# Performance work log

Hardware: AMD Instinct MI355X
Metric: run time of the kernel (lower is better)

## Reference

```python
import jax, jax.numpy as jnp
import numpy as np

N_NODES = 100000
N_EDGES = 1600000
MSG = 128
EPS = 1e-12  # F.normalize default eps


def setup_inputs() -> dict:
    key = jax.random.key(0)
    ks = jax.random.split(key, 12)
    s = 1.0 / np.sqrt(MSG)
    inp = {
        "x": jax.random.normal(ks[0], (N_NODES, 3), dtype=jnp.float32),
        "m_ij": jax.random.normal(ks[1], (N_EDGES, MSG), dtype=jnp.float32),
        "edges": jax.random.randint(ks[2], (2, N_EDGES), 0, N_NODES, dtype=jnp.int64),
        # weigths MLP: Linear(MSG,MSG) -> SiLU -> Linear(MSG,1)
        "Ww1": jax.random.uniform(ks[3], (MSG, MSG), jnp.float32, -s, s),
        "bw1": jax.random.uniform(ks[4], (MSG,), jnp.float32, -s, s),
        "Ww2": jax.random.uniform(ks[5], (MSG, 1), jnp.float32, -s, s),
        "bw2": jax.random.uniform(ks[6], (1,), jnp.float32, -s, s),
        # attention MLP: Linear(MSG,MSG) -> SiLU -> Linear(MSG,1)
        "Wa1": jax.random.uniform(ks[7], (MSG, MSG), jnp.float32, -s, s),
        "ba1": jax.random.uniform(ks[8], (MSG,), jnp.float32, -s, s),
        "Wa2": jax.random.uniform(ks[9], (MSG, 1), jnp.float32, -s, s),
        "ba2": jax.random.uniform(ks[10], (1,), jnp.float32, -s, s),
    }
    return inp


def reference(x, m_ij, edges, Ww1, bw1, Ww2, bw2, Wa1, ba1, Wa2, ba2):
    n_nodes = x.shape[0]
    src = edges[0]  # receiver index (scatter target)
    dst = edges[1]  # neighbor index

    # w_ij = MLP(m_ij) -> [E, 1]
    w_ij = jax.nn.silu(m_ij @ Ww1 + bw1) @ Ww2 + bw2

    # attention: a_ij = exp(MLP(m_ij)); normalized per receiver node (softmax-like)
    a_ij = jnp.exp(jax.nn.silu(m_ij @ Wa1 + ba1) @ Wa2 + ba2)  # [E, 1]
    a_i = jax.ops.segment_sum(a_ij, src, num_segments=n_nodes)  # [N, 1]
    w_ij = w_ij * (a_ij / a_i[src])

    # normalized position differences, weighted
    d = x[dst] - x[src]  # [E, 3]
    norm = jnp.maximum(jnp.linalg.norm(d, axis=1, keepdims=True), EPS)
    x_ij = (d / norm) * w_ij

    x_diff = jax.ops.segment_sum(x_ij, src, num_segments=n_nodes)  # [N, 3]
    return x + x_diff
```

## Files before the change

### kernel.cpp

```cpp
#include <hip/hip_runtime.h>
#include <cmath>

#define MSG 128
#define TILE 32
#define TPB 256
#define NB_MAX 768

typedef __attribute__((ext_vector_type(8))) __bf16 bf16x8;
typedef __attribute__((ext_vector_type(4))) float f32x4;

__device__ __forceinline__ unsigned short f2bf(float f) {
  union { float f; unsigned u; } v; v.f = f;
  unsigned r = v.u + 0x7FFFu + ((v.u >> 16) & 1u);
  return (unsigned short)(r >> 16);
}

__global__ void prep_weights_kernel(const float* __restrict__ Ww1,
                                    const float* __restrict__ Wa1,
                                    unsigned short* __restrict__ WtW,
                                    unsigned short* __restrict__ WtA) {
  int idx = blockIdx.x * blockDim.x + threadIdx.x;
  if (idx < MSG * MSG) {
    int k = idx >> 7;
    int n = idx & 127;
    WtW[n * MSG + k] = f2bf(Ww1[idx]);
    WtA[n * MSG + k] = f2bf(Wa1[idx]);
  }
}

__device__ __forceinline__ void gload_lds16(const float* g, float* l) {
  __builtin_amdgcn_global_load_lds(
      (const __attribute__((address_space(1))) void*)g,
      (__attribute__((address_space(3))) void*)l, 16, 0, 0);
}

__global__ __launch_bounds__(TPB, 3)
void edge_mlp_pipe_kernel(const float* __restrict__ m_ij,
                          const unsigned short* __restrict__ WtW,
                          const unsigned short* __restrict__ WtA,
                          const float* __restrict__ bw1, const float* __restrict__ Ww2,
                          const float* __restrict__ bw2,
                          const float* __restrict__ ba1, const float* __restrict__ Wa2,
                          const float* __restrict__ ba2,
                          const int* __restrict__ src,
                          const int* __restrict__ dst,
                          const float* __restrict__ x,
                          float* __restrict__ num4, int E, int ntiles) {
  __shared__ __align__(16) float buf[2][TILE * MSG];
  __shared__ float plds[2][4][TILE];

  const int tid = threadIdx.x;
  const int w = tid >> 6;
  const int lane = tid & 63;
  const int quad = lane >> 4;
  const int l16 = lane & 15;

  bf16x8 wf[2][2][4];
  f32x4 c1[2][2], c2[2][2];
  #pragma unroll
  for (int nt = 0; nt < 2; ++nt) {
    const int unit16 = w * 32 + nt * 16;
    const size_t ro = (size_t)(unit16 + l16) * MSG + quad * 8;
    #pragma unroll
    for (int kt = 0; kt < 4; ++kt) {
      wf[nt][0][kt] = *(const bf16x8*)(WtW + ro + kt * 32);
      wf[nt][1][kt] = *(const bf16x8*)(WtA + ro + kt * 32);
    }
    const int co = unit16 + quad * 4;
    c1[nt][0] = *(const f32x4*)(bw1 + co);
    c2[nt][0] = *(const f32x4*)(Ww2 + co);
    c1[nt][1] = *(const f32x4*)(ba1 + co);
    c2[nt][1] = *(const f32x4*)(Wa2 + co);
  }
  const float bw2s = bw2[0], ba2s = ba2[0];

  auto stage = [&](int tile, int bsel) {
    #pragma unroll
    for (int i = 0; i < 4; ++i) {
      const int chunk = i * TPB + tid;
      const int db = chunk * 16;
      const int row = db >> 9;
      const int col = db & 511;
      const int scol = col ^ ((row & 7) << 4);
      int grow = tile * TILE + row;
      if (grow >= E) grow = E - 1;
      gload_lds16(m_ij + (size_t)grow * MSG + (scol >> 2), &buf[bsel][0] + (db >> 2));
    }
  };

  const int fid = w * 8 + (lane & 7);

  int tt = blockIdx.x;
  int ge = tt * TILE + fid;
  bool vcur = (ge < E);
  int gec = vcur ? ge : 0;
  int sN = src[gec];
  int dN = dst[gec];
  asm volatile("" ::: "memory");
  stage(tt, 0);
  asm volatile("s_waitcnt vmcnt(4)" ::: "memory");
  float sx = x[3 * sN], sy = x[3 * sN + 1], sz = x[3 * sN + 2];
  float gx = x[3 * dN], gy = x[3 * dN + 1], gz = x[3 * dN + 2];
  asm volatile("s_waitcnt vmcnt(6)" ::: "memory");
  __builtin_amdgcn_s_barrier();
  int cur = 0;

  for (; tt < ntiles; tt += gridDim.x) {
    const int nxt = tt + (int)gridDim.x;
    const int snxt = (nxt < ntiles) ? nxt : (ntiles - 1);

    const int geN = snxt * TILE + fid;
    const bool vnxt = (geN < E);
    const int geNc = vnxt ? geN : 0;
    const int sN2 = src[geNc];
    const int dN2 = dst[geNc];
    asm volatile("" ::: "memory");
    stage(snxt, cur ^ 1);

    #pragma unroll
    for (int et = 0; et < 2; ++et) {
      const int row = et * 16 + l16;
      const int rbase = row * MSG;
      const int xorf = (row & 7) << 2;
      bf16x8 bfv[4];
      #pragma unroll
      for (int kt = 0; kt < 4; ++kt) {
        const int c0 = quad * 8 + kt * 32;
        const f32x4 v0 = *(const f32x4*)(&buf[cur][rbase + (c0 ^ xorf)]);
        const f32x4 v1 = *(const f32x4*)(&buf[cur][rbase + ((c0 + 4) ^ xorf)]);
        bf16x8 f;
        f[0] = (__bf16)v0.x; f[1] = (__bf16)v0.y;
        f[2] = (__bf16)v0.z; f[3] = (__bf16)v0.w;
        f[4] = (__bf16)v1.x; f[5] = (__bf16)v1.y;
        f[6] = (__bf16)v1.z; f[7] = (__bf16)v1.w;
        bfv[kt] = f;
      }
      f32x4 acc[2][2];
      #pragma unroll
      for (int nt = 0; nt < 2; ++nt) {
        acc[nt][0] = {0.f, 0.f, 0.f, 0.f};
        acc[nt][1] = {0.f, 0.f, 0.f, 0.f};
      }
      #pragma unroll
      for (int kt = 0; kt < 4; ++kt) {
        #pragma unroll
        for (int nt = 0; nt < 2; ++nt) {
          acc[nt][0] = __builtin_amdgcn_mfma_f32_16x16x32_bf16(wf[nt][0][kt], bfv[kt], acc[nt][0], 0, 0, 0);
          acc[nt][1] = __builtin_amdgcn_mfma_f32_16x16x32_bf16(wf[nt][1][kt], bfv[kt], acc[nt][1], 0, 0, 0);
        }
      }
      float pW = 0.f, pA = 0.f;
      #pragma unroll
      for (int nt = 0; nt < 2; ++nt) {
        #pragma unroll
        for (int r = 0; r < 4; ++r) {
          const float hw = acc[nt][0][r] + c1[nt][0][r];
          const float ha = acc[nt][1][r] + c1[nt][1][r];
          pW += (hw * c2[nt][0][r]) * __builtin_amdgcn_rcpf(1.f + __expf(-hw));
          pA += (ha * c2[nt][1][r]) * __builtin_amdgcn_rcpf(1.f + __expf(-ha));
        }
      }
      pW += __shfl_xor(pW, 16, 64); pW += __shfl_xor(pW, 32, 64);
      pA += __shfl_xor(pA, 16, 64); pA += __shfl_xor(pA, 32, 64);
      if (quad == 0) {
        plds[0][w][et * 16 + l16] = pW;
        plds[1][w][et * 16 + l16] = pA;
      }
    }

    asm volatile("s_waitcnt lgkmcnt(0)" ::: "memory");
    __builtin_amdgcn_s_barrier();

    asm volatile("s_waitcnt vmcnt(6)" ::: "memory");

    {
      float sW = 0.f, sA = 0.f;
      #pragma unroll
      for (int ww = 0; ww < 4; ++ww) {
        sW += plds[0][ww][fid];
        sA += plds[1][ww][fid];
      }
      const float a = __expf(sA + ba2s);
      const float t = (sW + bw2s) * a;
      const float dx = gx - sx, dy = gy - sy, dz = gz - sz;
      const float nrm = sqrtf(dx * dx + dy * dy + dz * dz);
      const float inv = t * __builtin_amdgcn_rcpf(fmaxf(nrm, 1e-12f));
      const float m = vcur ? 1.f : 0.f;
      if (quad == 0 && l16 < 8) {
        float* basep = num4 + (size_t)4 * sN;
        atomicAdd(basep + 0, dx * inv * m);
        atomicAdd(basep + 1, dy * inv * m);
        atomicAdd(basep + 2, dz * inv * m);
        atomicAdd(basep + 3, a * m);
      }
    }

    asm volatile("s_waitcnt vmcnt(8)" ::: "memory");
    const float sx2 = x[3 * sN2], sy2 = x[3 * sN2 + 1], sz2 = x[3 * sN2 + 2];
    const float gx2 = x[3 * dN2], gy2 = x[3 * dN2 + 1], gz2 = x[3 * dN2 + 2];

    asm volatile("s_waitcnt vmcnt(10) lgkmcnt(0)" ::: "memory");
    __builtin_amdgcn_s_barrier();

    sN = sN2; dN = dN2; vcur = vnxt;
    sx = sx2; sy = sy2; sz = sz2;
    gx = gx2; gy = gy2; gz = gz2;
    cur ^= 1;
  }
}

__global__ void finalize_kernel(const float* __restrict__ x,
                                const f32x4* __restrict__ num4,
                                float* __restrict__ out, int N) {
  int n = blockIdx.x * blockDim.x + threadIdx.x;
  if (n >= N) return;
  const f32x4 v = num4[n];
  const float inv = (v[3] != 0.f) ? __builtin_amdgcn_rcpf(v[3]) : 0.f;
  out[3 * n + 0] = x[3 * n + 0] + v[0] * inv;
  out[3 * n + 1] = x[3 * n + 1] + v[1] * inv;
  out[3 * n + 2] = x[3 * n + 2] + v[2] * inv;
}

extern "C" void kernel_launch(void* const* d_in, const int* in_sizes, int n_in,
                              void* d_out, int out_size, void* d_ws, size_t ws_size,
                              hipStream_t stream) {
  const float* x    = (const float*)d_in[0];
  const float* m_ij = (const float*)d_in[1];
  const int*   edges = (const int*)d_in[2];
  const float* Ww1 = (const float*)d_in[3];
  const float* bw1 = (const float*)d_in[4];
  const float* Ww2 = (const float*)d_in[5];
  const float* bw2 = (const float*)d_in[6];
  const float* Wa1 = (const float*)d_in[7];
  const float* ba1 = (const float*)d_in[8];
  const float* Wa2 = (const float*)d_in[9];
  const float* ba2 = (const float*)d_in[10];

  const int N = in_sizes[0] / 3;
  const int E = in_sizes[1] / MSG;
  const int* src = edges;
  const int* dst = edges + E;

  char* p = (char*)d_ws;
  unsigned short* WtW = (unsigned short*)p; p += (size_t)MSG * MSG * 2;
  unsigned short* WtA = (unsigned short*)p; p += (size_t)MSG * MSG * 2;
  float* num4 = (float*)p; p += (size_t)N * 4 * 4;

  float* out = (float*)d_out;

  const int ntiles = (E + TILE - 1) / TILE;
  const int nb = ntiles < NB_MAX ? ntiles : NB_MAX;

  hipMemsetAsync(num4, 0, (size_t)N * 4 * 4, stream);
  prep_weights_kernel<<<(MSG * MSG + 255) / 256, 256, 0, stream>>>(Ww1, Wa1, WtW, WtA);
  edge_mlp_pipe_kernel<<<nb, TPB, 0, stream>>>(
      m_ij, WtW, WtA, bw1, Ww2, bw2, ba1, Wa2, ba2, src, dst, x, num4, E, ntiles);
  finalize_kernel<<<(N + 255) / 256, 256, 0, stream>>>(x, (const f32x4*)num4, out, N);
}
```

Baseline: 1.204 ms.

## Software-pipeline MFMA and SiLU epilogue across tiles with triple-buffered LDS

Restructures the persistent edge loop so the MFMA for tile i runs after the barrier, while the SiLU/reduction epilogue of tile i-1 runs before it, and the node scatter is deferred by one iteration. LDS staging moves from double to triple buffering with a two-tile lookahead, and bias/second-layer weights move from registers to LDS. The aim is to overlap the transcendental-heavy epilogue with matrix work and memory latency and to hide more load latency. In exchange it uses more LDS and registers, which may lower occupancy, and the remaining vmcnt waits are loosely chosen.

```diff
diff --git a/kernel.cpp b/kernel.cpp
--- a/kernel.cpp
+++ b/kernel.cpp
@@ -46,35 +46,36 @@
                           const int* __restrict__ dst,
                           const float* __restrict__ x,
                           float* __restrict__ num4, int E, int ntiles) {
-  __shared__ __align__(16) float buf[2][TILE * MSG];
+  __shared__ __align__(16) float buf[3][TILE * MSG];
   __shared__ float plds[2][4][TILE];
+  __shared__ float clds[2][2][MSG];
 
   const int tid = threadIdx.x;
   const int w = tid >> 6;
   const int lane = tid & 63;
   const int quad = lane >> 4;
   const int l16 = lane & 15;
+  const int G = (int)gridDim.x;
+
+  for (int e = tid; e < 512; e += TPB) {
+    const int mat = e >> 8, c = (e >> 7) & 1, u = e & 127;
+    const float* s = (mat == 0) ? (c == 0 ? bw1 : Ww2) : (c == 0 ? ba1 : Wa2);
+    clds[mat][c][u] = s[u];
+  }
 
   bf16x8 wf[2][2][4];
-  f32x4 c1[2][2], c2[2][2];
   #pragma unroll
   for (int nt = 0; nt < 2; ++nt) {
-    const int unit16 = w * 32 + nt * 16;
-    const size_t ro = (size_t)(unit16 + l16) * MSG + quad * 8;
+    const size_t ro = (size_t)(w * 32 + nt * 16 + l16) * MSG + quad * 8;
     #pragma unroll
     for (int kt = 0; kt < 4; ++kt) {
       wf[nt][0][kt] = *(const bf16x8*)(WtW + ro + kt * 32);
       wf[nt][1][kt] = *(const bf16x8*)(WtA + ro + kt * 32);
     }
-    const int co = unit16 + quad * 4;
-    c1[nt][0] = *(const f32x4*)(bw1 + co);
-    c2[nt][0] = *(const f32x4*)(Ww2 + co);
-    c1[nt][1] = *(const f32x4*)(ba1 + co);
-    c2[nt][1] = *(const f32x4*)(Wa2 + co);
   }
   const float bw2s = bw2[0], ba2s = ba2[0];
 
-  auto stage = [&](int tile, int bsel) {
+  auto stage = [&](int tile, float* base) {
     #pragma unroll
     for (int i = 0; i < 4; ++i) {
       const int chunk = i * TPB + tid;
@@ -84,80 +85,69 @@
       const int scol = col ^ ((row & 7) << 4);
       int grow = tile * TILE + row;
       if (grow >= E) grow = E - 1;
-      gload_lds16(m_ij + (size_t)grow * MSG + (scol >> 2), &buf[bsel][0] + (db >> 2));
+      gload_lds16(m_ij + (size_t)grow * MSG + (scol >> 2), base + (db >> 2));
     }
   };
 
   const int fid = w * 8 + (lane & 7);
 
-  int tt = blockIdx.x;
-  int ge = tt * TILE + fid;
-  bool vcur = (ge < E);
-  int gec = vcur ? ge : 0;
-  int sN = src[gec];
-  int dN = dst[gec];
-  asm volatile("" ::: "memory");
-  stage(tt, 0);
-  asm volatile("s_waitcnt vmcnt(4)" ::: "memory");
-  float sx = x[3 * sN], sy = x[3 * sN + 1], sz = x[3 * sN + 2];
-  float gx = x[3 * dN], gy = x[3 * dN + 1], gz = x[3 * dN + 2];
-  asm volatile("s_waitcnt vmcnt(6)" ::: "memory");
-  __builtin_amdgcn_s_barrier();
-  int cur = 0;
-
-  for (; tt < ntiles; tt += gridDim.x) {
-    const int nxt = tt + (int)gridDim.x;
-    const int snxt = (nxt < ntiles) ? nxt : (ntiles - 1);
-
-    const int geN = snxt * TILE + fid;
-    const bool vnxt = (geN < E);
-    const int geNc = vnxt ? geN : 0;
+  int fsN[2] = {0, 0};
+  float fm[2] = {0.f, 0.f};
+  float fX[2][6];
+  #pragma unroll
+  for (int k = 0; k < 6; ++k) { fX[0][k] = 0.f; fX[1][k] = 0.f; }
+
+  f32x4 pacc[8];
+  #pragma unroll
+  for (int k = 0; k < 8; ++k) pacc[k] = {0.f, 0.f, 0.f, 0.f};
+
+  const int t0 = blockIdx.x;
+  {
+    int ge = t0 * TILE + fid;
+    bool v = (ge < E);
+    int gec = v ? ge : 0;
+    int sN = src[gec], dN = dst[gec];
+    stage(t0, &buf[0][0]);
+    { int t1 = t0 + G; if (t1 >= ntiles) t1 = ntiles - 1; stage(t1, &buf[1][0]); }
+    fsN[1] = sN; fm[1] = v ? 1.f : 0.f;
+    fX[1][0] = x[3 * sN]; fX[1][1] = x[3 * sN + 1]; fX[1][2] = x[3 * sN + 2];
+    fX[1][3] = x[3 * dN]; fX[1][4] = x[3 * dN + 1]; fX[1][5] = x[3 * dN + 2];
+    __syncthreads();
+  }
+
+  int p = 0;
+  int ci = 0;
+
+  for (int tt = t0; tt < ntiles; tt += G) {
+    int tn = tt + G;
+    const bool tnok = tn < ntiles;
+    const int tnc = tnok ? tn : ntiles - 1;
+    const int geN = tnc * TILE + fid;
+    const bool vN = tnok && (geN < E);
+    const int geNc = vN ? geN : 0;
     const int sN2 = src[geNc];
     const int dN2 = dst[geNc];
-    asm volatile("" ::: "memory");
-    stage(snxt, cur ^ 1);
+
+    { int ts = tt + 2 * G; if (ts >= ntiles) ts = ntiles - 1;
+      int sb = ci + 2; if (sb >= 3) sb -= 3;
+      stage(ts, &buf[sb][0]); }
 
     #pragma unroll
     for (int et = 0; et < 2; ++et) {
-      const int row = et * 16 + l16;
-      const int rbase = row * MSG;
-      const int xorf = (row & 7) << 2;
-      bf16x8 bfv[4];
-      #pragma unroll
-      for (int kt = 0; kt < 4; ++kt) {
-        const int c0 = quad * 8 + kt * 32;
-        const f32x4 v0 = *(const f32x4*)(&buf[cur][rbase + (c0 ^ xorf)]);
-        const f32x4 v1 = *(const f32x4*)(&buf[cur][rbase + ((c0 + 4) ^ xorf)]);
-        bf16x8 f;
-        f[0] = (__bf16)v0.x; f[1] = (__bf16)v0.y;
-        f[2] = (__bf16)v0.z; f[3] = (__bf16)v0.w;
-        f[4] = (__bf16)v1.x; f[5] = (__bf16)v1.y;
-        f[6] = (__bf16)v1.z; f[7] = (__bf16)v1.w;
-        bfv[kt] = f;
-      }
-      f32x4 acc[2][2];
-      #pragma unroll
-      for (int nt = 0; nt < 2; ++nt) {
-        acc[nt][0] = {0.f, 0.f, 0.f, 0.f};
-        acc[nt][1] = {0.f, 0.f, 0.f, 0.f};
-      }
-      #pragma unroll
-      for (int kt = 0; kt < 4; ++kt) {
-        #pragma unroll
-        for (int nt = 0; nt < 2; ++nt) {
-          acc[nt][0] = __builtin_amdgcn_mfma_f32_16x16x32_bf16(wf[nt][0][kt], bfv[kt], acc[nt][0], 0, 0, 0);
-          acc[nt][1] = __builtin_amdgcn_mfma_f32_16x16x32_bf16(wf[nt][1][kt], bfv[kt], acc[nt][1], 0, 0, 0);
-        }
-      }
       float pW = 0.f, pA = 0.f;
       #pragma unroll
       for (int nt = 0; nt < 2; ++nt) {
+        const int co = w * 32 + nt * 16 + quad * 4;
+        const f32x4 b1w = *(const f32x4*)&clds[0][0][co];
+        const f32x4 w2w = *(const f32x4*)&clds[0][1][co];
+        const f32x4 b1a = *(const f32x4*)&clds[1][0][co];
+        const f32x4 w2a = *(const f32x4*)&clds[1][1][co];
         #pragma unroll
         for (int r = 0; r < 4; ++r) {
-          const float hw = acc[nt][0][r] + c1[nt][0][r];
-          const float ha = acc[nt][1][r] + c1[nt][1][r];
-          pW += (hw * c2[nt][0][r]) * __builtin_amdgcn_rcpf(1.f + __expf(-hw));
-          pA += (ha * c2[nt][1][r]) * __builtin_amdgcn_rcpf(1.f + __expf(-ha));
+          const float hw = pacc[et * 4 + nt * 2 + 0][r] + b1w[r];
+          const float ha = pacc[et * 4 + nt * 2 + 1][r] + b1a[r];
+          pW += (hw * w2w[r]) * __builtin_amdgcn_rcpf(1.f + __expf(-hw));
+          pA += (ha * w2a[r]) * __builtin_amdgcn_rcpf(1.f + __expf(-ha));
         }
       }
       pW += __shfl_xor(pW, 16, 64); pW += __shfl_xor(pW, 32, 64);
@@ -171,41 +161,119 @@
     asm volatile("s_waitcnt lgkmcnt(0)" ::: "memory");
     __builtin_amdgcn_s_barrier();
 
-    asm volatile("s_waitcnt vmcnt(6)" ::: "memory");
-
     {
-      float sW = 0.f, sA = 0.f;
+      const float* bufc = &buf[ci][0];
       #pragma unroll
-      for (int ww = 0; ww < 4; ++ww) {
-        sW += plds[0][ww][fid];
-        sA += plds[1][ww][fid];
-      }
+      for (int et = 0; et < 2; ++et) {
+        const int row = et * 16 + l16;
+        const int rbase = row * MSG;
+        const int xorf = (row & 7) << 2;
+        bf16x8 bfv[4];
+        #pragma unroll
+        for (int kt = 0; kt < 4; ++kt) {
+          const int c0 = quad * 8 + kt * 32;
+          const f32x4 v0 = *(const f32x4*)(bufc + rbase + (c0 ^ xorf));
+          const f32x4 v1 = *(const f32x4*)(bufc + rbase + ((c0 + 4) ^ xorf));
+          bf16x8 f;
+          f[0] = (__bf16)v0.x; f[1] = (__bf16)v0.y;
+          f[2] = (__bf16)v0.z; f[3] = (__bf16)v0.w;
+          f[4] = (__bf16)v1.x; f[5] = (__bf16)v1.y;
+          f[6] = (__bf16)v1.z; f[7] = (__bf16)v1.w;
+          bfv[kt] = f;
+        }
+        f32x4 a0 = {0.f,0.f,0.f,0.f}, a1 = {0.f,0.f,0.f,0.f};
+        f32x4 a2 = {0.f,0.f,0.f,0.f}, a3 = {0.f,0.f,0.f,0.f};
+        #pragma unroll
+        for (int kt = 0; kt < 4; ++kt) {
+          a0 = __builtin_amdgcn_mfma_f32_16x16x32_bf16(wf[0][0][kt], bfv[kt], a0, 0, 0, 0);
+          a1 = __builtin_amdgcn_mfma_f32_16x16x32_bf16(wf[0][1][kt], bfv[kt], a1, 0, 0, 0);
+          a2 = __builtin_amdgcn_mfma_f32_16x16x32_bf16(wf[1][0][kt], bfv[kt], a2, 0, 0, 0);
+          a3 = __builtin_amdgcn_mfma_f32_16x16x32_bf16(wf[1][1][kt], bfv[kt], a3, 0, 0, 0);
+        }
+        pacc[et * 4 + 0] = a0;
+        pacc[et * 4 + 1] = a1;
+        pacc[et * 4 + 2] = a2;
+        pacc[et * 4 + 3] = a3;
+      }
+    }
+
+    {
+      float sW = plds[0][0][fid] + plds[0][1][fid] + plds[0][2][fid] + plds[0][3][fid];
+      float sA = plds[1][0][fid] + plds[1][1][fid] + plds[1][2][fid] + plds[1][3][fid];
       const float a = __expf(sA + ba2s);
       const float t = (sW + bw2s) * a;
-      const float dx = gx - sx, dy = gy - sy, dz = gz - sz;
+      const float dx = fX[p][3] - fX[p][0];
+      const float dy = fX[p][4] - fX[p][1];
+      const float dz = fX[p][5] - fX[p][2];
       const float nrm = sqrtf(dx * dx + dy * dy + dz * dz);
       const float inv = t * __builtin_amdgcn_rcpf(fmaxf(nrm, 1e-12f));
-      const float m = vcur ? 1.f : 0.f;
+      const float m = fm[p];
       if (quad == 0 && l16 < 8) {
-        float* basep = num4 + (size_t)4 * sN;
-        atomicAdd(basep + 0, dx * inv * m);
-        atomicAdd(basep + 1, dy * inv * m);
-        atomicAdd(basep + 2, dz * inv * m);
-        atomicAdd(basep + 3, a * m);
+        float* bp = num4 + (size_t)4 * fsN[p];
+        atomicAdd(bp + 0, dx * inv * m);
+        atomicAdd(bp + 1, dy * inv * m);
+        atomicAdd(bp + 2, dz * inv * m);
+        atomicAdd(bp + 3, a * m);
       }
     }
 
     asm volatile("s_waitcnt vmcnt(8)" ::: "memory");
-    const float sx2 = x[3 * sN2], sy2 = x[3 * sN2 + 1], sz2 = x[3 * sN2 + 2];
-    const float gx2 = x[3 * dN2], gy2 = x[3 * dN2 + 1], gz2 = x[3 * dN2 + 2];
-
-    asm volatile("s_waitcnt vmcnt(10) lgkmcnt(0)" ::: "memory");
+    fsN[p] = sN2; fm[p] = vN ? 1.f : 0.f;
+    fX[p][0] = x[3 * sN2]; fX[p][1] = x[3 * sN2 + 1]; fX[p][2] = x[3 * sN2 + 2];
+    fX[p][3] = x[3 * dN2]; fX[p][4] = x[3 * dN2 + 1]; fX[p][5] = x[3 * dN2 + 2];
+
+    asm volatile("s_waitcnt lgkmcnt(0)" ::: "memory");
     __builtin_amdgcn_s_barrier();
 
-    sN = sN2; dN = dN2; vcur = vnxt;
-    sx = sx2; sy = sy2; sz = sz2;
-    gx = gx2; gy = gy2; gz = gz2;
-    cur ^= 1;
+    p ^= 1;
+    ci = (ci == 2) ? 0 : ci + 1;
+  }
+
+  #pragma unroll
+  for (int et = 0; et < 2; ++et) {
+    float pW = 0.f, pA = 0.f;
+    #pragma unroll
+    for (int nt = 0; nt < 2; ++nt) {
+      const int co = w * 32 + nt * 16 + quad * 4;
+      const f32x4 b1w = *(const f32x4*)&clds[0][0][co];
+      const f32x4 w2w = *(const f32x4*)&clds[0][1][co];
+      const f32x4 b1a = *(const f32x4*)&clds[1][0][co];
+      const f32x4 w2a = *(const f32x4*)&clds[1][1][co];
+      #pragma unroll
+      for (int r = 0; r < 4; ++r) {
+        const float hw = pacc[et * 4 + nt * 2 + 0][r] + b1w[r];
+        const float ha = pacc[et * 4 + nt * 2 + 1][r] + b1a[r];
+        pW += (hw * w2w[r]) * __builtin_amdgcn_rcpf(1.f + __expf(-hw));
+        pA += (ha * w2a[r]) * __builtin_amdgcn_rcpf(1.f + __expf(-ha));
+      }
+    }
+    pW += __shfl_xor(pW, 16, 64); pW += __shfl_xor(pW, 32, 64);
+    pA += __shfl_xor(pA, 16, 64); pA += __shfl_xor(pA, 32, 64);
+    if (quad == 0) {
+      plds[0][w][et * 16 + l16] = pW;
+      plds[1][w][et * 16 + l16] = pA;
+    }
+  }
+  asm volatile("s_waitcnt lgkmcnt(0)" ::: "memory");
+  __builtin_amdgcn_s_barrier();
+  {
+    float sW = plds[0][0][fid] + plds[0][1][fid] + plds[0][2][fid] + plds[0][3][fid];
+    float sA = plds[1][0][fid] + plds[1][1][fid] + plds[1][2][fid] + plds[1][3][fid];
+    const float a = __expf(sA + ba2s);
+    const float t = (sW + bw2s) * a;
+    const float dx = fX[p][3] - fX[p][0];
+    const float dy = fX[p][4] - fX[p][1];
+    const float dz = fX[p][5] - fX[p][2];
+    const float nrm = sqrtf(dx * dx + dy * dy + dz * dz);
+    const float inv = t * __builtin_amdgcn_rcpf(fmaxf(nrm, 1e-12f));
+    const float m = fm[p];
+    if (quad == 0 && l16 < 8) {
+      float* bp = num4 + (size_t)4 * fsN[p];
+      atomicAdd(bp + 0, dx * inv * m);
+      atomicAdd(bp + 1, dy * inv * m);
+      atomicAdd(bp + 2, dz * inv * m);
+      atomicAdd(bp + 3, a * m);
+    }
   }
 }
 
```

New measurement: 2.427 ms. +101.6%, slower.
